# Performance work log

Hardware: AMD Instinct MI355X
Metric: run time of the kernel (lower is better)

The kernel has to match this reference:

```python
import jax, jax.numpy as jnp
import numpy as np

N_NODES = 100000
N_EDGES = 1600000
N_GRAPHS = 256
D_IN = 128
D_HID = 128
D_OUT = 64


def graph_conv(x, src, dst, W_rel, b_rel, W_root):
    # PyG GraphConv: out = lin_rel(mean_{j->i} x_j) + lin_root(x)
    msgs = jax.ops.segment_sum(x[src], dst, num_segments=N_NODES)  # [N, d]
    deg = jax.ops.segment_sum(jnp.ones((src.shape[0],), x.dtype), dst, num_segments=N_NODES)
    agg = msgs / jnp.maximum(deg, 1.0)[:, None]
    return agg @ W_rel + b_rel + x @ W_root


def setup_inputs() -> dict:
    key = jax.random.key(0)
    ks = jax.random.split(key, 12)
    x = jax.random.normal(ks[0], (N_NODES, D_IN), dtype=jnp.float32)
    edge_index = jax.random.randint(ks[1], (2, N_EDGES), 0, N_NODES, dtype=jnp.int64)
    batch = jnp.sort(jax.random.randint(ks[2], (N_NODES,), 0, N_GRAPHS, dtype=jnp.int64))
    def lin(k, fan_in, fan_out):
        bound = 1.0 / np.sqrt(fan_in)
        return jax.random.uniform(k, (fan_in, fan_out), jnp.float32, -bound, bound)
    inp = {
        "x": x, "edge_index": edge_index, "batch": batch,
        "W1_rel": lin(ks[3], D_IN, D_HID), "b1_rel": jnp.zeros((D_HID,), jnp.float32), "W1_root": lin(ks[4], D_IN, D_HID),
        "W2_rel": lin(ks[5], D_HID, D_HID), "b2_rel": jnp.zeros((D_HID,), jnp.float32), "W2_root": lin(ks[6], D_HID, D_HID),
        "W3_rel": lin(ks[7], D_HID, D_HID), "b3_rel": jnp.zeros((D_HID,), jnp.float32), "W3_root": lin(ks[8], D_HID, D_HID),
        "Wl": lin(ks[9], D_HID, D_OUT), "bl": jnp.zeros((D_OUT,), jnp.float32),
    }
    return inp


def reference(x, edge_index, batch, W1_rel, b1_rel, W1_root, W2_rel, b2_rel, W2_root,
              W3_rel, b3_rel, W3_root, Wl, bl):
    src, dst = edge_index[0], edge_index[1]
    h = jax.nn.relu(graph_conv(x, src, dst, W1_rel, b1_rel, W1_root))
    h = jax.nn.relu(graph_conv(h, src, dst, W2_rel, b2_rel, W2_root))
    h = graph_conv(h, src, dst, W3_rel, b3_rel, W3_root)
    # global mean pool over graphs
    sums = jax.ops.segment_sum(h, batch, num_segments=N_GRAPHS)          # [G, d]
    cnts = jax.ops.segment_sum(jnp.ones((h.shape[0],), h.dtype), batch, num_segments=N_GRAPHS)
    pooled = sums / jnp.maximum(cnts, 1.0)[:, None]
    # dropout is identity at inference
    return pooled @ Wl + bl  # [G, D_OUT]
```

## Files before the change

kernel.cpp:

```cpp
#include <hip/hip_runtime.h>
#include <hip/hip_bf16.h>

#define N_NODES  100000
#define N_EDGES  1600000
#define N_GRAPHS 256
#define DCH      128
#define DOUT     64
#define NB       391
#define PADB     512
#define SLACK    4608
#define CHUNK    2048
#define NBINA    782

typedef short v8s __attribute__((ext_vector_type(8)));
typedef float v4f __attribute__((ext_vector_type(4)));

static __device__ __forceinline__ float bf2f(unsigned short u) {
    unsigned int x = ((unsigned int)u) << 16;
    return __builtin_bit_cast(float, x);
}
static __device__ __forceinline__ unsigned short f2bf(float f) {
    unsigned int x = __builtin_bit_cast(unsigned int, f);
    unsigned int r = (x + 0x7fffu + ((x >> 16) & 1u)) >> 16;
    return (unsigned short)r;
}
static __device__ __forceinline__ int clampi(int v, int lo, int hi) {
    return v < lo ? lo : (v > hi ? hi : v);
}

__global__ void __launch_bounds__(256) binAprep_kernel(
    const int* __restrict__ src, const int* __restrict__ dst,
    int* __restrict__ gcur, uint2* __restrict__ region,
    const float* __restrict__ x, unsigned short* __restrict__ B2,
    const float* __restrict__ W1rel, const float* __restrict__ W1root,
    const float* __restrict__ W2rel, const float* __restrict__ W2root,
    const float* __restrict__ W3rel, const float* __restrict__ W3root,
    unsigned short* __restrict__ frag,
    unsigned short* __restrict__ z1, unsigned short* __restrict__ z2)
{
    __shared__ uint2 stage[CHUNK];
    __shared__ int hcnt[PADB], hcnt2[PADB], hoff[PADB], garr[PADB];
    __shared__ int s2[256];
    int tid = threadIdx.x;

    if (blockIdx.x >= NBINA) {
        int bid = blockIdx.x - NBINA;
        if (bid < 12500) {
            size_t i = ((size_t)bid * 256 + tid) * 4;
            float4 f = *reinterpret_cast<const float4*>(x + i);
            uint2 o;
            o.x = ((unsigned)f2bf(f.y) << 16) | (unsigned)f2bf(f.x);
            o.y = ((unsigned)f2bf(f.w) << 16) | (unsigned)f2bf(f.z);
            *reinterpret_cast<uint2*>(B2 + i) = o;
        } else if (bid < 12548) {
            int gid = (bid - 12500) * 256 + tid;
            int lane = gid & 63;
            int nt   = (gid >> 6) & 7;
            int kt   = (gid >> 9) & 7;
            int L    = gid >> 12;
            const float* rel  = (L == 0) ? W1rel  : (L == 1) ? W2rel  : W3rel;
            const float* root = (L == 0) ? W1root : (L == 1) ? W2root : W3root;
            int n  = nt * 16 + (lane & 15);
            int k0 = kt * 32 + (lane >> 4) * 8;
            unsigned short o[8];
            #pragma unroll
            for (int j = 0; j < 8; j++) {
                int k = k0 + j;
                float w = (k < 128) ? rel[k * 128 + n] : root[(k - 128) * 128 + n];
                o[j] = f2bf(w);
            }
            uint4 u;
            u.x = (unsigned)o[0] | ((unsigned)o[1] << 16);
            u.y = (unsigned)o[2] | ((unsigned)o[3] << 16);
            u.z = (unsigned)o[4] | ((unsigned)o[5] << 16);
            u.w = (unsigned)o[6] | ((unsigned)o[7] << 16);
            *reinterpret_cast<uint4*>(frag + (size_t)gid * 8) = u;
        } else {
            if (tid < 64)       reinterpret_cast<unsigned*>(z1)[tid] = 0;
            else if (tid < 128) reinterpret_cast<unsigned*>(z2)[tid - 64] = 0;
        }
        return;
    }

    int e0  = blockIdx.x * CHUNK;
    int nedge = N_EDGES - e0; if (nedge > CHUNK) nedge = CHUNK;

    for (int b = tid; b < PADB; b += 256) { hcnt[b] = 0; hcnt2[b] = 0; }
    __syncthreads();

    int es[CHUNK / 256], ed[CHUNK / 256];
    #pragma unroll
    for (int j = 0; j < CHUNK / 256; j++) {
        int e = e0 + j * 256 + tid;
        if (e < N_EDGES) {
            es[j] = clampi(src[e], 0, N_NODES - 1);
            ed[j] = clampi(dst[e], 0, N_NODES - 1);
            atomicAdd(&hcnt[ed[j] >> 8], 1);
        } else { es[j] = -1; ed[j] = 0; }
    }
    __syncthreads();

    int v0 = hcnt[2 * tid], v1 = hcnt[2 * tid + 1];
    s2[tid] = v0 + v1; __syncthreads();
    for (int off = 1; off < 256; off <<= 1) {
        int xx = (tid >= off) ? s2[tid - off] : 0;
        __syncthreads();
        s2[tid] += xx;
        __syncthreads();
    }
    int excl = s2[tid] - (v0 + v1);
    hoff[2 * tid] = excl; hoff[2 * tid + 1] = excl + v0;
    __syncthreads();

    for (int b = tid; b < NB; b += 256) {
        int c = hcnt[b];
        garr[b] = b * SLACK + ((c > 0) ? atomicAdd(&gcur[b], c) : 0);
    }
    __syncthreads();

    #pragma unroll
    for (int j = 0; j < CHUNK / 256; j++) {
        if (es[j] >= 0) {
            int b = ed[j] >> 8;
            int pos = atomicAdd(&hcnt2[b], 1) + hoff[b];
            stage[pos] = (uint2){(unsigned)es[j], (unsigned)ed[j]};
        }
    }
    __syncthreads();

    for (int i = tid; i < nedge; i += 256) {
        uint2 en = stage[i];
        int b = (int)(en.y >> 8);
        int gpos = garr[b] + (i - hoff[b]);
        if (gpos < (b + 1) * SLACK) region[gpos] = en;
    }
}

__global__ void __launch_bounds__(256) binFinish_kernel(const uint2* __restrict__ region, const int* __restrict__ gcur,
                                                        int* __restrict__ rowptr, int* __restrict__ csr) {
    __shared__ int h[256], sc[256], cur[256], s2[256], hoff[PADB];
    int b = blockIdx.x, tid = threadIdx.x;
    int c0 = gcur[2 * tid];     if (c0 > SLACK) c0 = SLACK;
    int c1 = gcur[2 * tid + 1]; if (c1 > SLACK) c1 = SLACK;
    s2[tid] = c0 + c1;
    h[tid] = 0;
    __syncthreads();
    for (int off = 1; off < 256; off <<= 1) {
        int xx = (tid >= off) ? s2[tid - off] : 0;
        __syncthreads();
        s2[tid] += xx;
        __syncthreads();
    }
    int excl = s2[tid] - (c0 + c1);
    hoff[2 * tid] = excl; hoff[2 * tid + 1] = excl + c0;
    __syncthreads();
    if (b == 0 && tid == 255) rowptr[N_NODES] = s2[255];
    int base = hoff[b];
    int size = gcur[b]; if (size > SLACK) size = SLACK;
    int node0 = b * 256;
    for (int j = tid; j < size; j += 256) {
        unsigned loc = region[b * SLACK + j].y - (unsigned)node0;
        if (loc < 256u) atomicAdd(&h[loc], 1);
    }
    __syncthreads();
    int v = h[tid]; sc[tid] = v; __syncthreads();
    for (int off = 1; off < 256; off <<= 1) {
        int xx = (tid >= off) ? sc[tid - off] : 0;
        __syncthreads();
        sc[tid] += xx;
        __syncthreads();
    }
    int myptr = base + sc[tid] - v;
    int node = node0 + tid;
    if (node < N_NODES) rowptr[node] = myptr;
    cur[tid] = myptr;
    __syncthreads();
    for (int j = tid; j < size; j += 256) {
        uint2 en = region[b * SLACK + j];
        unsigned loc = en.y - (unsigned)node0;
        if (loc < 256u) {
            int p = atomicAdd(&cur[loc], 1);
            if (p >= 0 && p < N_EDGES) csr[p] = (int)en.x;
        }
    }
}

__global__ void __launch_bounds__(256, 8) agg_kernel(
    const unsigned short* __restrict__ hin,
    const int* __restrict__ rowptr, const int* __restrict__ csr,
    unsigned short* __restrict__ agg)
{
    const int wid  = __builtin_amdgcn_readfirstlane(threadIdx.x >> 6);
    const int lane = threadIdx.x & 63;
    const int l16  = lane & 15;
    const int node = blockIdx.x * 4 + wid;
    const int r0 = rowptr[node];
    const int r1 = rowptr[node + 1];

    float a0 = 0.f, a1 = 0.f;
    int t = csr[r0 + l16];
    for (int c = r0; c < r1; c += 16) {
        int tn = csr[c + 16 + l16];
        int idx = (c + l16 < r1) ? t : N_NODES;
        #pragma unroll
        for (int j = 0; j < 16; j++) {
            int s = __builtin_amdgcn_readlane(idx, j);
            unsigned v = *reinterpret_cast<const unsigned*>(hin + (size_t)s * DCH + lane * 2);
            a0 += bf2f((unsigned short)(v & 0xffffu));
            a1 += bf2f((unsigned short)(v >> 16));
        }
        t = tn;
    }
    int deg = r1 - r0;
    float inv = 1.0f / (float)(deg > 1 ? deg : 1);
    unsigned o = ((unsigned)f2bf(a1 * inv) << 16) | (unsigned)f2bf(a0 * inv);
    *reinterpret_cast<unsigned*>(agg + (size_t)node * DCH + lane * 2) = o;
}

__global__ void __launch_bounds__(256, 4) gemm_kernel(
    unsigned short* agg,
    const unsigned short* __restrict__ root,
    const unsigned short* __restrict__ frag, const float* __restrict__ bias,
    const int* __restrict__ batch, float* __restrict__ psum, int mode)
{
    __shared__ __attribute__((aligned(16))) unsigned short As[4][16 * DCH];
    const int wave = threadIdx.x >> 6;
    const int lane = threadIdx.x & 63;
    const int l16  = lane & 15;
    const int quad = lane >> 4;
    const int base = blockIdx.x * 64 + wave * 16;
    if (base >= N_NODES) return;

    char* Asb = reinterpret_cast<char*>(As[wave]);

    #pragma unroll
    for (int k = 0; k < 4; k++) {
        const char* gp = reinterpret_cast<const char*>(agg) + (size_t)base * 256 + k * 1024 + lane * 16;
        uint4 d = *reinterpret_cast<const uint4*>(gp);
        int row = k * 4 + (lane >> 4);
        int col = (lane & 15) * 16;
        *reinterpret_cast<uint4*>(Asb + row * 256 + (col ^ ((row & 7) << 4))) = d;
    }

    v4f acc[8];
    #pragma unroll
    for (int nt = 0; nt < 8; nt++) acc[nt] = (v4f){0.f, 0.f, 0.f, 0.f};

    #pragma unroll
    for (int kt = 0; kt < 8; kt++) {
        v8s av;
        if (kt < 4) {
            int co = (kt * 64 + quad * 16) ^ ((l16 & 7) << 4);
            av = *reinterpret_cast<const v8s*>(Asb + l16 * 256 + co);
        } else {
            int ak = (kt - 4) * 32 + quad * 8;
            av = *reinterpret_cast<const v8s*>(root + (size_t)(base + l16) * DCH + ak);
        }
        #pragma unroll
        for (int nt = 0; nt < 8; nt++) {
            v8s b = *reinterpret_cast<const v8s*>(frag + (((size_t)(kt * 8 + nt)) * 64 + lane) * 8);
            acc[nt] = __builtin_amdgcn_mfma_f32_16x16x32_bf16(av, b, acc[nt], 0, 0, 0);
        }
    }

    if (mode != 2) {
        #pragma unroll
        for (int nt = 0; nt < 8; nt++) {
            int n = nt * 16 + l16;
            float bv = bias[n];
            #pragma unroll
            for (int r = 0; r < 4; r++) {
                int row = base + quad * 4 + r;
                float v = acc[nt][r] + bv;
                if (mode == 1) v = fmaxf(v, 0.f);
                agg[(size_t)row * DCH + n] = f2bf(v);
            }
        }
    } else {
        bool fast = (batch[base] == batch[base + 15]);
        if (fast) {
            int g = batch[base];
            #pragma unroll
            for (int nt = 0; nt < 8; nt++) {
                int n = nt * 16 + l16;
                float s = acc[nt][0] + acc[nt][1] + acc[nt][2] + acc[nt][3] + 4.0f * bias[n];
                s += __shfl_xor(s, 16);
                s += __shfl_xor(s, 32);
                if (quad == 0) atomicAdd(&psum[g * DCH + n], s);
            }
        } else {
            int g[4];
            #pragma unroll
            for (int r = 0; r < 4; r++) g[r] = batch[base + quad * 4 + r];
            #pragma unroll
            for (int nt = 0; nt < 8; nt++) {
                int n = nt * 16 + l16;
                float bv = bias[n];
                float s = 0.f; int cg = -1;
                #pragma unroll
                for (int r = 0; r < 4; r++) {
                    if (g[r] != cg) {
                        if (cg >= 0) atomicAdd(&psum[cg * DCH + n], s);
                        s = 0.f; cg = g[r];
                    }
                    s += acc[nt][r] + bv;
                }
                if (cg >= 0) atomicAdd(&psum[cg * DCH + n], s);
            }
        }
    }
}

static __device__ __forceinline__ int lowerb(const int* __restrict__ a, int n, int key) {
    int lo = 0, hi = n;
    while (lo < hi) { int mid = (lo + hi) >> 1; if (a[mid] < key) lo = mid + 1; else hi = mid; }
    return lo;
}

__global__ void __launch_bounds__(64) final_kernel(const float* __restrict__ psum,
                                                   const int* __restrict__ batch,
                                                   const float* __restrict__ Wl, const float* __restrict__ bl,
                                                   float* __restrict__ out) {
    __shared__ float ps[DCH];
    __shared__ int bounds[2];
    int g = blockIdx.x, tid = threadIdx.x;
    if (tid == 0) {
        bounds[0] = lowerb(batch, N_NODES, g);
        bounds[1] = lowerb(batch, N_NODES, g + 1);
    }
    __syncthreads();
    int cnt = bounds[1] - bounds[0];
    float inv = 1.0f / (float)(cnt > 1 ? cnt : 1);
    ps[tid] = psum[g * DCH + tid] * inv;
    ps[tid + 64] = psum[g * DCH + tid + 64] * inv;
    __syncthreads();
    float o = 0.f;
    #pragma unroll 4
    for (int c = 0; c < DCH; c++) o += ps[c] * Wl[c * DOUT + tid];
    out[g * DOUT + tid] = o + bl[tid];
}

extern "C" void kernel_launch(void* const* d_in, const int* in_sizes, int n_in,
                              void* d_out, int out_size, void* d_ws, size_t ws_size,
                              hipStream_t stream) {
    const float* x     = (const float*)d_in[0];
    const int*   edge  = (const int*)d_in[1];
    const int*   src   = edge;
    const int*   dst   = edge + N_EDGES;
    const int*   batch = (const int*)d_in[2];
    const float* W1rel  = (const float*)d_in[3];
    const float* b1     = (const float*)d_in[4];
    const float* W1root = (const float*)d_in[5];
    const float* W2rel  = (const float*)d_in[6];
    const float* b2     = (const float*)d_in[7];
    const float* W2root = (const float*)d_in[8];
    const float* W3rel  = (const float*)d_in[9];
    const float* b3     = (const float*)d_in[10];
    const float* W3root = (const float*)d_in[11];
    const float* Wl     = (const float*)d_in[12];
    const float* bl     = (const float*)d_in[13];
    float* out = (float*)d_out;

    char* ws = (char*)d_ws;
    size_t off = 0;
    auto carve = [&](size_t bytes) -> void* {
        void* p = ws + off;
        off += (bytes + 255) & ~(size_t)255;
        return p;
    };
    int*            rowptr  = (int*)carve((size_t)(N_NODES + 1) * 4);
    int*            csr     = (int*)carve((size_t)(N_EDGES + 64) * 4);
    int*            gcur    = (int*)carve((size_t)PADB * 4 + (size_t)N_GRAPHS * DCH * 4);
    float*          psum    = (float*)(gcur + PADB);
    unsigned short* frag    = (unsigned short*)carve((size_t)3 * 8 * 8 * 64 * 8 * 2);
    unsigned short* B1      = (unsigned short*)carve((size_t)(N_NODES + 1) * DCH * 2);
    unsigned short* B2      = (unsigned short*)carve((size_t)(N_NODES + 1) * DCH * 2);
    uint2*          region  = (uint2*)B1;

    hipMemsetAsync(gcur, 0, (size_t)PADB * 4 + (size_t)N_GRAPHS * DCH * 4, stream);

    binAprep_kernel<<<NBINA + 12549, 256, 0, stream>>>(src, dst, gcur, region,
                                                       x, B2, W1rel, W1root, W2rel, W2root, W3rel, W3root,
                                                       frag, B1 + (size_t)N_NODES * DCH, B2 + (size_t)N_NODES * DCH);
    binFinish_kernel<<<NB, 256, 0, stream>>>(region, gcur, rowptr, csr);

    const int aggGrid  = N_NODES / 4;
    const int gemmGrid = (N_NODES + 63) / 64;

    agg_kernel<<<aggGrid, 256, 0, stream>>>(B2, rowptr, csr, B1);
    gemm_kernel<<<gemmGrid, 256, 0, stream>>>(B1, B2, frag,         b1, batch, psum, 1);
    agg_kernel<<<aggGrid, 256, 0, stream>>>(B1, rowptr, csr, B2);
    gemm_kernel<<<gemmGrid, 256, 0, stream>>>(B2, B1, frag + 32768, b2, batch, psum, 1);
    agg_kernel<<<aggGrid, 256, 0, stream>>>(B2, rowptr, csr, B1);
    gemm_kernel<<<gemmGrid, 256, 0, stream>>>(B1, B2, frag + 65536, b3, batch, psum, 2);

    final_kernel<<<N_GRAPHS, 64, 0, stream>>>(psum, batch, Wl, bl, out);
}
```

Baseline: 419.8 us.

## Fuse neighbor aggregation and GEMM into one per-layer kernel

```diff
diff --git a/kernel.cpp b/kernel.cpp
--- a/kernel.cpp
+++ b/kernel.cpp
@@ -185,67 +185,51 @@
     }
 }
 
-__global__ void __launch_bounds__(256, 8) agg_kernel(
+__global__ void __launch_bounds__(256, 6) layer_kernel(
     const unsigned short* __restrict__ hin,
     const int* __restrict__ rowptr, const int* __restrict__ csr,
-    unsigned short* __restrict__ agg)
-{
-    const int wid  = __builtin_amdgcn_readfirstlane(threadIdx.x >> 6);
-    const int lane = threadIdx.x & 63;
-    const int l16  = lane & 15;
-    const int node = blockIdx.x * 4 + wid;
-    const int r0 = rowptr[node];
-    const int r1 = rowptr[node + 1];
-
-    float a0 = 0.f, a1 = 0.f;
-    int t = csr[r0 + l16];
-    for (int c = r0; c < r1; c += 16) {
-        int tn = csr[c + 16 + l16];
-        int idx = (c + l16 < r1) ? t : N_NODES;
-        #pragma unroll
-        for (int j = 0; j < 16; j++) {
-            int s = __builtin_amdgcn_readlane(idx, j);
-            unsigned v = *reinterpret_cast<const unsigned*>(hin + (size_t)s * DCH + lane * 2);
-            a0 += bf2f((unsigned short)(v & 0xffffu));
-            a1 += bf2f((unsigned short)(v >> 16));
-        }
-        t = tn;
-    }
-    int deg = r1 - r0;
-    float inv = 1.0f / (float)(deg > 1 ? deg : 1);
-    unsigned o = ((unsigned)f2bf(a1 * inv) << 16) | (unsigned)f2bf(a0 * inv);
-    *reinterpret_cast<unsigned*>(agg + (size_t)node * DCH + lane * 2) = o;
-}
-
-__global__ void __launch_bounds__(256, 4) gemm_kernel(
-    unsigned short* agg,
-    const unsigned short* __restrict__ root,
     const unsigned short* __restrict__ frag, const float* __restrict__ bias,
+    unsigned short* __restrict__ hout,
     const int* __restrict__ batch, float* __restrict__ psum, int mode)
 {
-    __shared__ __attribute__((aligned(16))) unsigned short As[4][16 * DCH];
+    __shared__ __attribute__((aligned(16))) unsigned short As[16 * DCH];
     const int wave = threadIdx.x >> 6;
     const int lane = threadIdx.x & 63;
     const int l16  = lane & 15;
     const int quad = lane >> 4;
-    const int base = blockIdx.x * 64 + wave * 16;
-    if (base >= N_NODES) return;
-
-    char* Asb = reinterpret_cast<char*>(As[wave]);
+    const int base = blockIdx.x * 16;
+    char* Asb = reinterpret_cast<char*>(As);
 
     #pragma unroll
     for (int k = 0; k < 4; k++) {
-        const char* gp = reinterpret_cast<const char*>(agg) + (size_t)base * 256 + k * 1024 + lane * 16;
-        uint4 d = *reinterpret_cast<const uint4*>(gp);
-        int row = k * 4 + (lane >> 4);
-        int col = (lane & 15) * 16;
-        *reinterpret_cast<uint4*>(Asb + row * 256 + (col ^ ((row & 7) << 4))) = d;
-    }
-
-    v4f acc[8];
-    #pragma unroll
-    for (int nt = 0; nt < 8; nt++) acc[nt] = (v4f){0.f, 0.f, 0.f, 0.f};
-
+        const int row  = wave * 4 + k;
+        const int node = base + row;
+        const int r0 = rowptr[node];
+        const int r1 = rowptr[node + 1];
+        float a0 = 0.f, a1 = 0.f;
+        int t = csr[r0 + l16];
+        for (int c = r0; c < r1; c += 16) {
+            int tn = csr[c + 16 + l16];
+            int idx = (c + l16 < r1) ? t : N_NODES;
+            #pragma unroll
+            for (int j = 0; j < 16; j++) {
+                int s = __builtin_amdgcn_readlane(idx, j);
+                unsigned v = *reinterpret_cast<const unsigned*>(hin + (size_t)s * DCH + lane * 2);
+                a0 += bf2f((unsigned short)(v & 0xffffu));
+                a1 += bf2f((unsigned short)(v >> 16));
+            }
+            t = tn;
+        }
+        int deg = r1 - r0;
+        float inv = 1.0f / (float)(deg > 1 ? deg : 1);
+        unsigned o = ((unsigned)f2bf(a1 * inv) << 16) | (unsigned)f2bf(a0 * inv);
+        *reinterpret_cast<unsigned*>(Asb + row * 256 + ((lane * 4) ^ ((row & 7) << 4))) = o;
+    }
+    __syncthreads();
+
+    const int nt0 = wave * 2;
+    v4f acc0 = (v4f){0.f, 0.f, 0.f, 0.f};
+    v4f acc1 = (v4f){0.f, 0.f, 0.f, 0.f};
     #pragma unroll
     for (int kt = 0; kt < 8; kt++) {
         v8s av;
@@ -254,58 +238,61 @@
             av = *reinterpret_cast<const v8s*>(Asb + l16 * 256 + co);
         } else {
             int ak = (kt - 4) * 32 + quad * 8;
-            av = *reinterpret_cast<const v8s*>(root + (size_t)(base + l16) * DCH + ak);
-        }
-        #pragma unroll
-        for (int nt = 0; nt < 8; nt++) {
-            v8s b = *reinterpret_cast<const v8s*>(frag + (((size_t)(kt * 8 + nt)) * 64 + lane) * 8);
-            acc[nt] = __builtin_amdgcn_mfma_f32_16x16x32_bf16(av, b, acc[nt], 0, 0, 0);
-        }
-    }
+            av = *reinterpret_cast<const v8s*>(hin + (size_t)(base + l16) * DCH + ak);
+        }
+        v8s b0 = *reinterpret_cast<const v8s*>(frag + (((size_t)(kt * 8 + nt0)) * 64 + lane) * 8);
+        v8s b1 = *reinterpret_cast<const v8s*>(frag + (((size_t)(kt * 8 + nt0 + 1)) * 64 + lane) * 8);
+        acc0 = __builtin_amdgcn_mfma_f32_16x16x32_bf16(av, b0, acc0, 0, 0, 0);
+        acc1 = __builtin_amdgcn_mfma_f32_16x16x32_bf16(av, b1, acc1, 0, 0, 0);
+    }
+
+    const int n0 = nt0 * 16 + l16;
+    const int n1 = n0 + 16;
+    const float bv0 = bias[n0];
+    const float bv1 = bias[n1];
 
     if (mode != 2) {
         #pragma unroll
-        for (int nt = 0; nt < 8; nt++) {
-            int n = nt * 16 + l16;
-            float bv = bias[n];
-            #pragma unroll
-            for (int r = 0; r < 4; r++) {
-                int row = base + quad * 4 + r;
-                float v = acc[nt][r] + bv;
-                if (mode == 1) v = fmaxf(v, 0.f);
-                agg[(size_t)row * DCH + n] = f2bf(v);
-            }
+        for (int r = 0; r < 4; r++) {
+            int row = base + quad * 4 + r;
+            float x0 = acc0[r] + bv0;
+            float x1 = acc1[r] + bv1;
+            if (mode == 1) { x0 = fmaxf(x0, 0.f); x1 = fmaxf(x1, 0.f); }
+            hout[(size_t)row * DCH + n0] = f2bf(x0);
+            hout[(size_t)row * DCH + n1] = f2bf(x1);
         }
     } else {
         bool fast = (batch[base] == batch[base + 15]);
         if (fast) {
             int g = batch[base];
-            #pragma unroll
-            for (int nt = 0; nt < 8; nt++) {
-                int n = nt * 16 + l16;
-                float s = acc[nt][0] + acc[nt][1] + acc[nt][2] + acc[nt][3] + 4.0f * bias[n];
-                s += __shfl_xor(s, 16);
-                s += __shfl_xor(s, 32);
-                if (quad == 0) atomicAdd(&psum[g * DCH + n], s);
+            float s0 = acc0[0] + acc0[1] + acc0[2] + acc0[3] + 4.0f * bv0;
+            float s1 = acc1[0] + acc1[1] + acc1[2] + acc1[3] + 4.0f * bv1;
+            s0 += __shfl_xor(s0, 16); s0 += __shfl_xor(s0, 32);
+            s1 += __shfl_xor(s1, 16); s1 += __shfl_xor(s1, 32);
+            if (quad == 0) {
+                atomicAdd(&psum[g * DCH + n0], s0);
+                atomicAdd(&psum[g * DCH + n1], s1);
             }
         } else {
             int g[4];
             #pragma unroll
             for (int r = 0; r < 4; r++) g[r] = batch[base + quad * 4 + r];
+            float s0 = 0.f, s1 = 0.f; int cg = -1;
             #pragma unroll
-            for (int nt = 0; nt < 8; nt++) {
-                int n = nt * 16 + l16;
-                float bv = bias[n];
-                float s = 0.f; int cg = -1;
-                #pragma unroll
-                for (int r = 0; r < 4; r++) {
-                    if (g[r] != cg) {
-                        if (cg >= 0) atomicAdd(&psum[cg * DCH + n], s);
-                        s = 0.f; cg = g[r];
+            for (int r = 0; r < 4; r++) {
+                if (g[r] != cg) {
+                    if (cg >= 0) {
+                        atomicAdd(&psum[cg * DCH + n0], s0);
+                        atomicAdd(&psum[cg * DCH + n1], s1);
                     }
-                    s += acc[nt][r] + bv;
+                    s0 = 0.f; s1 = 0.f; cg = g[r];
                 }
-                if (cg >= 0) atomicAdd(&psum[cg * DCH + n], s);
+                s0 += acc0[r] + bv0;
+                s1 += acc1[r] + bv1;
+            }
+            if (cg >= 0) {
+                atomicAdd(&psum[cg * DCH + n0], s0);
+                atomicAdd(&psum[cg * DCH + n1], s1);
             }
         }
     }
@@ -384,15 +371,11 @@
                                                        frag, B1 + (size_t)N_NODES * DCH, B2 + (size_t)N_NODES * DCH);
     binFinish_kernel<<<NB, 256, 0, stream>>>(region, gcur, rowptr, csr);
 
-    const int aggGrid  = N_NODES / 4;
-    const int gemmGrid = (N_NODES + 63) / 64;
-
-    agg_kernel<<<aggGrid, 256, 0, stream>>>(B2, rowptr, csr, B1);
-    gemm_kernel<<<gemmGrid, 256, 0, stream>>>(B1, B2, frag,         b1, batch, psum, 1);
-    agg_kernel<<<aggGrid, 256, 0, stream>>>(B1, rowptr, csr, B2);
-    gemm_kernel<<<gemmGrid, 256, 0, stream>>>(B2, B1, frag + 32768, b2, batch, psum, 1);
-    agg_kernel<<<aggGrid, 256, 0, stream>>>(B2, rowptr, csr, B1);
-    gemm_kernel<<<gemmGrid, 256, 0, stream>>>(B1, B2, frag + 65536, b3, batch, psum, 2);
+    const int layerGrid = N_NODES / 16;
+
+    layer_kernel<<<layerGrid, 256, 0, stream>>>(B2, rowptr, csr, frag,         b1, B1, batch, psum, 1);
+    layer_kernel<<<layerGrid, 256, 0, stream>>>(B1, rowptr, csr, frag + 32768, b2, B2, batch, psum, 1);
+    layer_kernel<<<layerGrid, 256, 0, stream>>>(B2, rowptr, csr, frag + 65536, b3, B1, batch, psum, 2);
 
     final_kernel<<<N_GRAPHS, 64, 0, stream>>>(psum, batch, Wl, bl, out);
 }
```

Measured after the change: 387.6 us. 1.08x faster.
